# Kernel tuning notes

Hardware: AMD Instinct MI355X
Metric: run time of the kernel (lower is better)

The kernel has to match this reference:

```python
import jax, jax.numpy as jnp
import numpy as np

B, N, L = 32, 50, 16384  # batch, n_templates, segment length
KT = 4096                # template kernel length


def conv1d(x, w, pad, groups=1):
    # x: [B, Cin, L], w: [Cout, Cin/groups, K] (torch layout)
    return jax.lax.conv_general_dilated(
        x, w, window_strides=(1,), padding=[(pad, pad)],
        dimension_numbers=('NCH', 'OIH', 'NCH'), feature_group_count=groups)


def maxpool3(x):
    # MaxPool1d(kernel=3, stride=3), floor mode (VALID)
    return jax.lax.reduce_window(x, -jnp.inf, jax.lax.max,
                                 (1, 1, 3), (1, 1, 3), 'VALID')


def pad_to(x, m):
    p = (-x.shape[-1]) % m
    pads = ((0, 0),) * (x.ndim - 1) + ((0, p),)
    return jnp.pad(x, pads)


def setup_inputs() -> dict:
    key = jax.random.key(0)
    ks = jax.random.split(key, 12)
    return dict(
        xi=jax.random.normal(ks[0], (B, 2, L), jnp.float32),
        S_t_m12=jax.random.normal(ks[1], (2, 1, L), jnp.float32) * 0.01,
        template=jax.random.normal(ks[2], (N, 2, KT), jnp.float32) * 0.01,
        hh_sqrt=jax.random.uniform(ks[3], (N, 2), jnp.float32) + 0.5,
        W1=jax.random.normal(ks[4], (16, 2, 3), jnp.float32) * 0.1,
        b1=jnp.zeros((16,), jnp.float32),
        W2=jax.random.normal(ks[5], (32, 16, 3), jnp.float32) * 0.1,
        b2=jnp.zeros((32,), jnp.float32),
        W3=jax.random.normal(ks[6], (32, 128), jnp.float32) * 0.1,
        b3=jnp.zeros((32,), jnp.float32),
        W4=jax.random.normal(ks[7], (2, 32), jnp.float32) * 0.1,
        b4=jnp.zeros((2,), jnp.float32),
    )


def reference(xi, S_t_m12, template, hh_sqrt, W1, b1, W2, b2, W3, b3, W4, b4):
    # Whitening matched filter: grouped conv with kernel length L
    y = conv1d(xi, S_t_m12, L - 1, groups=2)          # [B, 2, 2L-1]
    y = pad_to(y, L)                                   # [B, 2, 2L]
    # wrap-fold each channel: reshape(B,2,L).sum over the fold axis
    d_SA = y[:, 0].reshape(-1, 2, L).sum(1)[:, None, :]  # [B,1,L]
    d_SE = y[:, 1].reshape(-1, 2, L).sum(1)[:, None, :]
    h_SA = template[:, 0, :].reshape(-1, 1, KT)          # [N,1,KT]
    h_SE = template[:, 1, :].reshape(-1, 1, KT)
    dh_A = pad_to(conv1d(d_SA, h_SA, KT - 1), L).reshape(-1, N, 2, L).sum(2)  # [B,N,L]
    dh_E = pad_to(conv1d(d_SE, h_SE, KT - 1), L).reshape(-1, N, 2, L).sum(2)
    z = jnp.stack((dh_A, dh_E), -1).transpose(0, 2, 1, 3)  # [B,L,N,2]
    z = z / hh_sqrt                                         # broadcast [N,2]
    z = z.max(axis=1).transpose(0, 2, 1)                    # [B,2,N]
    # small CNN + MLP head
    h = maxpool3(jax.nn.sigmoid(conv1d(z, W1, 0) + b1[None, :, None]))  # [B,16,16]
    h = maxpool3(jax.nn.sigmoid(conv1d(h, W2, 0) + b2[None, :, None]))  # [B,32,4]
    h = h.reshape(h.shape[0], -1)                                        # [B,128]
    h = jax.nn.relu(h @ W3.T + b3)
    return h @ W4.T + b4                                                 # [B,2]
```

## Files before the change

kernel.cpp:

```cpp
#include <hip/hip_runtime.h>
#include <math.h>

#define L_LEN 16384
#define M_LEN 8192
#define KT_LEN 4096
#define BB 32
#define NTPL 50
#define SPEC_STRIDE 8224
#define NSIG 166
#define NTF 1024
#define NTI 512
#define PI_F 3.14159265358979323846f
#define C8 0.92387953251128674f
#define S8 0.38268343236508978f
#define R2_F 0.70710678118654752f

typedef float cf2 __attribute__((ext_vector_type(2)));


__device__ __forceinline__ cf2 cmul(cf2 a, cf2 b) {
    cf2 t, d;
    asm("v_pk_mul_f32 %0, %1, %2 op_sel:[0,0] op_sel_hi:[0,1]"
        : "=v"(t) : "v"(a), "v"(b));
    asm("v_pk_fma_f32 %0, %1, %2, %3 op_sel:[1,1,0] op_sel_hi:[1,0,1] neg_lo:[0,1,0]"
        : "=v"(d) : "v"(a), "v"(b), "v"(t));
    return d;
}
__device__ __forceinline__ cf2 cmulc(cf2 a, cf2 b) {
    cf2 t, d;
    asm("v_pk_mul_f32 %0, %1, %2 op_sel:[0,0] op_sel_hi:[0,1] neg_hi:[0,1]"
        : "=v"(t) : "v"(a), "v"(b));
    asm("v_pk_fma_f32 %0, %1, %2, %3 op_sel:[1,1,0] op_sel_hi:[1,0,1]"
        : "=v"(d) : "v"(a), "v"(b), "v"(t));
    return d;
}
__device__ __forceinline__ cf2 cmulca(cf2 a, cf2 b) {
    cf2 t, d;
    asm("v_pk_mul_f32 %0, %1, %2 op_sel:[0,0] op_sel_hi:[0,1]"
        : "=v"(t) : "v"(a), "v"(b));
    asm("v_pk_fma_f32 %0, %1, %2, %3 op_sel:[1,1,0] op_sel_hi:[1,0,1] neg_hi:[1,0,0]"
        : "=v"(d) : "v"(a), "v"(b), "v"(t));
    return d;
}
__device__ __forceinline__ cf2 pk_addch(cf2 a, cf2 b) {
    cf2 d;
    asm("v_pk_add_f32 %0, %1, %2 neg_hi:[0,1]" : "=v"(d) : "v"(a), "v"(b));
    return d;
}
__device__ __forceinline__ cf2 pk_subcl(cf2 a, cf2 b) {
    cf2 d;
    asm("v_pk_add_f32 %0, %1, %2 neg_lo:[0,1]" : "=v"(d) : "v"(a), "v"(b));
    return d;
}
__device__ __forceinline__ cf2 pk_compose1(cf2 s, cf2 r) {
    cf2 d;
    asm("v_pk_add_f32 %0, %1, %2 op_sel:[0,1] op_sel_hi:[0,0] neg_lo:[0,1]"
        : "=v"(d) : "v"(s), "v"(r));
    return d;
}
__device__ __forceinline__ cf2 pk_compose2(cf2 s, cf2 r) {
    cf2 d;
    asm("v_pk_add_f32 %0, %1, %2 op_sel:[0,1] op_sel_hi:[0,0] neg_hi:[1,0]"
        : "=v"(d) : "v"(s), "v"(r));
    return d;
}
template<int SIGN>
__device__ __forceinline__ cf2 rot90(cf2 z) {
    return (SIGN < 0) ? (cf2){z.y, -z.x} : (cf2){-z.y, z.x};
}
template<int SIGN>
__device__ __forceinline__ cf2 ldT(const cf2* __restrict__ T, int idx) {
    cf2 t = T[idx];
    if (SIGN > 0) t.y = -t.y;
    return t;
}

__device__ __forceinline__ int swz(int i) { return i ^ (((i >> 5) & 15) << 1); }

__device__ __forceinline__ int pos8(int f) {
    return ((f & 7) << 10) | (((f >> 3) & 7) << 7) |
           (((f >> 6) & 7) << 4) | (((f >> 9) & 7) << 1) | ((f >> 12) & 1);
}

template<int SIGN>
__device__ __forceinline__ void dft16(cf2 x[16]) {
    const float S = (SIGN < 0) ? -1.f : 1.f;
    const cf2 w1 = {0.9238795325112867f, S * 0.3826834323650898f};
    const cf2 w2 = {0.7071067811865476f, S * 0.7071067811865476f};
    const cf2 w3 = {0.3826834323650898f, S * 0.9238795325112867f};
    cf2 v[16];
    #pragma unroll
    for (int n1 = 0; n1 < 4; ++n1) {
        cf2 a0 = x[n1], a1 = x[n1+4], a2 = x[n1+8], a3 = x[n1+12];
        cf2 t0 = a0 + a2, t2 = a0 - a2;
        cf2 t1 = a1 + a3, t3 = rot90<SIGN>(a1 - a3);
        cf2 u0 = t0 + t1, u1 = t2 + t3;
        cf2 u2 = t0 - t1, u3 = t2 - t3;
        if (n1 == 1) { u1 = cmul(u1, w1); u2 = cmul(u2, w2); u3 = cmul(u3, w3); }
        else if (n1 == 2) { u1 = cmul(u1, w2); u2 = rot90<SIGN>(u2);
                            u3 = rot90<SIGN>(cmul(u3, w2)); }
        else if (n1 == 3) { u1 = cmul(u1, w3); u2 = rot90<SIGN>(cmul(u2, w2));
                            u3 = -cmul(u3, w1); }
        v[0*4+n1] = u0; v[1*4+n1] = u1; v[2*4+n1] = u2; v[3*4+n1] = u3;
    }
    #pragma unroll
    for (int r = 0; r < 4; ++r) {
        cf2 a0 = v[r*4+0], a1 = v[r*4+1], a2 = v[r*4+2], a3 = v[r*4+3];
        cf2 t0 = a0 + a2, t2 = a0 - a2;
        cf2 t1 = a1 + a3, t3 = rot90<SIGN>(a1 - a3);
        x[r]    = t0 + t1; x[r+4]  = t2 + t3;
        x[r+8]  = t0 - t1; x[r+12] = t2 - t3;
    }
}

template<int SIGN>
__device__ __forceinline__ void butterfly16(cf2* A, const int idx[16], cf2 w1) {
    cf2 x[16];
    #pragma unroll
    for (int n = 0; n < 16; ++n) x[n] = A[idx[n]];
    dft16<SIGN>(x);
    A[idx[0]] = x[0];
    A[idx[1]] = cmul(x[1], w1);
    const cf2 w2 = cmul(w1, w1);
    A[idx[2]] = cmul(x[2], w2);
    const cf2 w3 = cmul(w1, w2);
    A[idx[3]] = cmul(x[3], w3);
    const cf2 w4 = cmul(w2, w2);
    A[idx[4]] = cmul(x[4], w4);
    A[idx[5]] = cmul(x[5], cmul(w1, w4));
    A[idx[6]] = cmul(x[6], cmul(w2, w4));
    A[idx[7]] = cmul(x[7], cmul(w3, w4));
    const cf2 w8 = cmul(w4, w4);
    A[idx[8]]  = cmul(x[8],  w8);
    A[idx[9]]  = cmul(x[9],  cmul(w1, w8));
    A[idx[10]] = cmul(x[10], cmul(w2, w8));
    A[idx[11]] = cmul(x[11], cmul(w3, w8));
    const cf2 w12 = cmul(w4, w8);
    A[idx[12]] = cmul(x[12], w12);
    A[idx[13]] = cmul(x[13], cmul(w1, w12));
    A[idx[14]] = cmul(x[14], cmul(w2, w12));
    A[idx[15]] = cmul(x[15], cmul(w3, w12));
}

template<int SIGN>
__device__ __forceinline__ void dft8(cf2 x[8]) {
    const cf2 w81 = { R2_F, SIGN * R2_F };
    const cf2 w83 = { -R2_F, SIGN * R2_F };
    cf2 u0 = x[0] + x[4], u1 = x[1] + x[5], u2 = x[2] + x[6], u3 = x[3] + x[7];
    cf2 v0 = x[0] - x[4];
    cf2 v1 = cmul(x[1] - x[5], w81);
    cf2 v2 = rot90<SIGN>(x[2] - x[6]);
    cf2 v3 = cmul(x[3] - x[7], w83);
    cf2 t0 = u0 + u2, t2 = u0 - u2;
    cf2 t1 = u1 + u3, t3 = rot90<SIGN>(u1 - u3);
    x[0] = t0 + t1; x[2] = t2 + t3; x[4] = t0 - t1; x[6] = t2 - t3;
    cf2 s0 = v0 + v2, s2 = v0 - v2;
    cf2 s1 = v1 + v3, s3 = rot90<SIGN>(v1 - v3);
    x[1] = s0 + s1; x[3] = s2 + s3; x[5] = s0 - s1; x[7] = s2 - s3;
}

template<int SIGN>
__device__ __forceinline__ void butterfly8(cf2* A, const int idx[8], cf2 w1) {
    cf2 x[8];
    #pragma unroll
    for (int n = 0; n < 8; ++n) x[n] = A[idx[n]];
    dft8<SIGN>(x);
    A[idx[0]] = x[0];
    A[idx[1]] = cmul(x[1], w1);
    const cf2 w2 = cmul(w1, w1);
    A[idx[2]] = cmul(x[2], w2);
    const cf2 w3 = cmul(w1, w2);
    A[idx[3]] = cmul(x[3], w3);
    const cf2 w4 = cmul(w2, w2);
    A[idx[4]] = cmul(x[4], w4);
    A[idx[5]] = cmul(x[5], cmul(w1, w4));
    A[idx[6]] = cmul(x[6], cmul(w2, w4));
    A[idx[7]] = cmul(x[7], cmul(w3, w4));
}

__global__ __launch_bounds__(NTF, 4)
void fwd_fft_kernel(const float* __restrict__ xi, const float* __restrict__ w,
                    const float* __restrict__ tmpl, cf2* __restrict__ Tw,
                    cf2* __restrict__ spec) {
    __shared__ __attribute__((aligned(16))) cf2 A[M_LEN];
    const int sig = blockIdx.x;
    const int tid = threadIdx.x;

    if (sig >= NSIG) {
        const int k = (sig - NSIG) * NTF + tid;
        const int quad = k >> 12, mm = k & 4095;
        float s, c; __sincosf(PI_F * (float)mm / 8192.f, &s, &c);
        cf2 v;
        if      (quad == 0) v = (cf2){ c, -s};
        else if (quad == 1) v = (cf2){-s, -c};
        else if (quad == 2) v = (cf2){-c,  s};
        else                v = (cf2){ s,  c};
        Tw[k] = v;
        return;
    }

    const float* src;
    int nre;
    if (sig < 64)      { src = xi   + sig * L_LEN;         nre = L_LEN; }
    else if (sig < 66) { src = w    + (sig - 64) * L_LEN;  nre = L_LEN; }
    else               { src = tmpl + (sig - 66) * KT_LEN; nre = KT_LEN; }
    const bool isW = (sig >= 64 && sig < 66);
    const int nc = nre >> 1;
    const float4* s4 = (const float4*)src;
    const int g0 = tid ^ ((tid >> 4) & 15);
    #pragma unroll
    for (int m = 0; m < 4; ++m) {
        const int u = 2*tid + 2048*m;
        float4 vv = (u < nc) ? s4[tid + 1024*m] : make_float4(0.f, 0.f, 0.f, 0.f);
        ((float4*)A)[g0 + 1024*m] = vv;
    }
    __syncthreads();

    {
        int idx[8]; const int b0 = swz(tid);
        #pragma unroll
        for (int n = 0; n < 8; ++n) idx[n] = b0 + 1024*n;
        float sn, cs; __sincosf(-PI_F * (float)(2*tid) / 8192.f, &sn, &cs);
        butterfly8<-1>(A, idx, (cf2){cs, sn});
    }
    __syncthreads();
    {
        const int blk = tid >> 7, j = tid & 127, jb = blk*1024;
        const int jsw = j ^ (((j >> 5) & 3) << 1);
        int idx[8];
        #pragma unroll
        for (int n = 0; n < 8; ++n) idx[n] = jb + 128*n + (jsw ^ ((n & 3) << 3));
        float sn, cs; __sincosf(-PI_F * (float)(16*j) / 8192.f, &sn, &cs);
        butterfly8<-1>(A, idx, (cf2){cs, sn});
    }
    __syncthreads();
    {
        const int blk = tid >> 4, j = tid & 15;
        const int base = blk*128 + j, bx = (blk & 3) << 3;
        int idx[8];
        #pragma unroll
        for (int n = 0; n < 8; ++n) idx[n] = (base + 16*n) ^ bx ^ ((n >> 1) << 1);
        float sn, cs; __sincosf(-PI_F * (float)(128*j) / 8192.f, &sn, &cs);
        butterfly8<-1>(A, idx, (cf2){cs, sn});
    }
    __syncthreads();
    {
        const int blk = tid >> 1, j = tid & 1;
        const int Xa = ((blk >> 1) & 15) << 1;
        const int base = ((blk << 4) | j) ^ (Xa & 16);
        const int xv = Xa & 14;
        int idx[8];
        #pragma unroll
        for (int n = 0; n < 8; ++n) idx[n] = base + ((2*n) ^ xv);
        cf2 w1 = j ? (cf2){C8, -S8} : (cf2){1.f, 0.f};
        butterfly8<-1>(A, idx, w1);
    }
    __syncthreads();
    #pragma unroll
    for (int m = 0; m < 4; ++m) {
        float4 pq = ((float4*)A)[g0 + 1024*m];
        ((float4*)A)[g0 + 1024*m] = make_float4(pq.x + pq.z, pq.y + pq.w,
                                                pq.x - pq.z, pq.y - pq.w);
    }
    __syncthreads();

    cf2* out = spec + (size_t)sig * SPEC_STRIDE;
    #pragma unroll
    for (int m = 0; m < 8; ++m) {
        const int f = tid + 1024*m;
        const int fb = (M_LEN - f) & (M_LEN - 1);
        cf2 Za = A[swz(pos8(f))];
        cf2 Zb = A[swz(pos8(fb))];
        cf2 E = (cf2){0.5f*(Za.x + Zb.x), 0.5f*(Za.y - Zb.y)};
        cf2 D = (cf2){Za.x - Zb.x, Za.y + Zb.y};
        cf2 O = (cf2){0.5f*D.y, -0.5f*D.x};
        float sn, cs;
        __sincosf(-PI_F * (float)f / 8192.f, &sn, &cs);
        cf2 val = E + (cf2){cs*O.x - sn*O.y, cs*O.y + sn*O.x};
        if (isW) {
            const int k = (4094 * f) & (L_LEN - 1);
            float psn, pcs; __sincosf(-PI_F * (float)k / 8192.f, &psn, &pcs);
            val = cmul((cf2){val.x, -val.y}, (cf2){pcs, psn});
        }
        out[f] = val;
    }
    if (tid == 0) {
        cf2 Za = A[swz(0)];
        cf2 val = (cf2){Za.x - Za.y, 0.f};
        if (isW) {
            val = (cf2){-val.x, 0.f};
        }
        out[M_LEN] = val;
    }
}

__global__ __launch_bounds__(1024)
void xv_kernel(cf2* __restrict__ spec) {
    const int bc = blockIdx.x;
    cf2* Xs = spec + (size_t)bc * SPEC_STRIDE;
    const cf2* Vs = spec + (size_t)(64 + (bc & 1)) * SPEC_STRIDE;
    const int tid = threadIdx.x;
    float4* X4 = (float4*)Xs;
    const float4* V4 = (const float4*)Vs;
    #pragma unroll
    for (int m = 0; m < 4; ++m) {
        const int p = tid + 1024*m;
        float4 xv = X4[p], vv = V4[p];
        cf2 a = cmul((cf2){xv.x, xv.y}, (cf2){vv.x, vv.y});
        cf2 b = cmul((cf2){xv.z, xv.w}, (cf2){vv.z, vv.w});
        X4[p] = make_float4(a.x, a.y, b.x, b.y);
    }
    if (tid == 0) Xs[M_LEN] = cmul(Xs[M_LEN], Vs[M_LEN]);
}

__global__ __launch_bounds__(NTI, 4)
void inv_fft_kernel(const cf2* __restrict__ spec, const cf2* __restrict__ T,
                    const float* __restrict__ hh, float* __restrict__ zarr) {
    __shared__ __attribute__((aligned(16))) cf2 A[M_LEN];
    const int idx0 = blockIdx.x;
    const int c = idx0 & 1;
    const int n = (idx0 >> 1) % NTPL;
    const int b = idx0 / (2 * NTPL);
    const int tid = threadIdx.x;

    const cf2* Xs = spec + (size_t)(b*2 + c)      * SPEC_STRIDE;
    const cf2* Hs = spec + (size_t)(66 + n*2 + c) * SPEC_STRIDE;
    const float4* X4 = (const float4*)Xs;
    const float4* H4 = (const float4*)Hs;
    const float4* T4 = (const float4*)T;

    #pragma unroll
    for (int m = 0; m < 2; ++m) {
        const int tp = tid + 512*m;
        const int f0 = 2*tp, f1 = f0 + 1;
        float4 xa = X4[tp],        ha = H4[tp];
        float4 xq = X4[tp + 2048], hq = H4[tp + 2048];
        cf2 PA0 = cmulc((cf2){xa.x, xa.y}, (cf2){ha.x, ha.y});
        cf2 PA1 = cmulc((cf2){xa.z, xa.w}, (cf2){ha.z, ha.w});
        cf2 QB0 = cmulc((cf2){xq.x, xq.y}, (cf2){hq.x, hq.y});
        cf2 QB1 = cmulc((cf2){xq.z, xq.w}, (cf2){hq.z, hq.w});
        cf2 PB0 = cmulc(Xs[4096 - f0], Hs[4096 - f0]);
        cf2 PB1 = cmulc(Xs[4096 - f1], Hs[4096 - f1]);
        cf2 QA0 = cmulc(Xs[8192 - f0], Hs[8192 - f0]);
        cf2 QA1 = cmulc(Xs[8192 - f1], Hs[8192 - f1]);
        float4 tf4 = T4[tp];
        float4 t2a = T4[2*tp];
        float4 t2b = T4[2*tp + 1];
        cf2 Tf0 = (cf2){tf4.x, tf4.y}, Tf1 = (cf2){tf4.z, tf4.w};
        cf2 T20 = (cf2){t2a.x, t2a.y}, T21 = (cf2){t2b.x, t2b.y};
        cf2 SpA0 = pk_addch(PA0, QA0), SmA0 = pk_subcl(PA0, QA0);
        cf2 RA0 = cmulca(Tf0, SmA0);
        cf2 ZA1_0 = pk_compose1(SpA0, RA0);
        cf2 ZA2_0 = pk_compose2(SpA0, RA0);
        cf2 tB0 = (cf2){-Tf0.y, -Tf0.x};
        cf2 SpB0 = pk_addch(PB0, QB0), SmB0 = pk_subcl(PB0, QB0);
        cf2 RB0 = cmulca(tB0, SmB0);
        cf2 ZB1_0 = pk_compose1(SpB0, RB0);
        cf2 ZB2_0 = pk_compose2(SpB0, RB0);
        cf2 top0 = ZA1_0 + ZB2_0;
        cf2 bot0 = cmulca(T20, ZA1_0 - ZB2_0);
        cf2 SpA1 = pk_addch(PA1, QA1), SmA1 = pk_subcl(PA1, QA1);
        cf2 RA1 = cmulca(Tf1, SmA1);
        cf2 ZA1_1 = pk_compose1(SpA1, RA1);
        cf2 ZA2_1 = pk_compose2(SpA1, RA1);
        cf2 tB1 = (cf2){-Tf1.y, -Tf1.x};
        cf2 SpB1 = pk_addch(PB1, QB1), SmB1 = pk_subcl(PB1, QB1);
        cf2 RB1 = cmulca(tB1, SmB1);
        cf2 ZB1_1 = pk_compose1(SpB1, RB1);
        cf2 ZB2_1 = pk_compose2(SpB1, RB1);
        cf2 top1 = ZA1_1 + ZB2_1;
        cf2 bot1 = cmulca(T21, ZA1_1 - ZB2_1);
        const int gt = tp ^ ((tp >> 4) & 15);
        ((float4*)A)[gt]        = make_float4(top0.x, top0.y, top1.x, top1.y);
        ((float4*)A)[2048 + gt] = make_float4(bot0.x, bot0.y, bot1.x, bot1.y);
        if (tp > 0) {
            cf2 tr0 = ZB1_0 + ZA2_0;
            cf2 dr0 = cmul(ZB1_0 - ZA2_0, T20);
            A[swz(4096 - f0)] = tr0;
            A[swz(8192 - f0)] = -dr0;
        }
        cf2 tr1 = ZB1_1 + ZA2_1;
        cf2 dr1 = cmul(ZB1_1 - ZA2_1, T21);
        A[swz(4096 - f1)] = tr1;
        A[swz(8192 - f1)] = -dr1;
    }
    if (tid == 0) {
        cf2 P = cmulc(Xs[2048], Hs[2048]);
        cf2 Q = cmulc(Xs[6144], Hs[6144]);
        cf2 Tc = (cf2){R2_F, -R2_F};
        cf2 Sp = pk_addch(P, Q), Sm = pk_subcl(P, Q);
        cf2 R = cmulca(Tc, Sm);
        cf2 Z1 = pk_compose1(Sp, R), Z2 = pk_compose2(Sp, R);
        cf2 d = Z1 - Z2;
        A[swz(2048)] = Z1 + Z2;
        A[swz(6144)] = (cf2){-d.y, d.x};
    }
    __syncthreads();

    {
        const int h = tid >> 8, j = tid & 255;
        const int Hb = h << 12;
        const int jx = j ^ (((j >> 5) & 7) << 1);
        int idx[16];
        #pragma unroll
        for (int nn = 0; nn < 16; ++nn)
            idx[nn] = Hb + 256*nn + (jx ^ ((nn & 1) << 4));
        butterfly16<+1>(A, idx, ldT<+1>(T, 4*j));
    }
    __syncthreads();
    {
        const int h = tid >> 8, q = (tid >> 4) & 15, j = tid & 15;
        const int base = (h << 12) + (q << 8);
        const int qb = q & 1;
        int idx[16];
        #pragma unroll
        for (int nn = 0; nn < 16; ++nn)
            idx[nn] = base + 16*(nn ^ qb) + (j ^ (((nn >> 1) & 7) << 1));
        butterfly16<+1>(A, idx, ldT<+1>(T, 64*j));
    }
    __syncthreads();

    float mx = -INFINITY;
    {
        const int bb = 16 * (tid ^ ((tid >> 4) & 1));
        const int m3 = ((tid >> 1) & 7) << 1;
        cf2 x[16];
        #pragma unroll
        for (int e = 0; e < 8; ++e) {
            float4 v = ((const float4*)A)[(bb + ((2*e) ^ m3)) >> 1];
            x[2*e]     = (cf2){v.x, v.y};
            x[2*e + 1] = (cf2){v.z, v.w};
        }
        dft16<+1>(x);
        #pragma unroll
        for (int nn = 0; nn < 16; ++nn)
            mx = fmaxf(mx, fmaxf(x[nn].x, x[nn].y));
    }
    __syncthreads();
    for (int off = 32; off > 0; off >>= 1)
        mx = fmaxf(mx, __shfl_xor(mx, off));
    const int lane = tid & 63, wv = tid >> 6;
    float* redf = (float*)A;
    if (lane == 0) redf[wv] = mx;
    __syncthreads();
    if (tid == 0) {
        float mm = redf[0];
        for (int i = 1; i < NTI/64; ++i) mm = fmaxf(mm, redf[i]);
        zarr[(b*2 + c)*NTPL + n] = mm / (2.f * (float)M_LEN * hh[n*2 + c]);
    }
}

#define W1_OFF 0
#define B1_OFF 96
#define W2_OFF 112
#define B2_OFF 1648
#define W3_OFF 1680
#define B3_OFF 5904
#define W4_OFF 5936
#define B4_OFF 6000
#define WSM_SZ 6002

__global__ __launch_bounds__(256)
void head_kernel(const float* __restrict__ zarr,
                 const float* __restrict__ W1, const float* __restrict__ b1,
                 const float* __restrict__ W2, const float* __restrict__ b2,
                 const float* __restrict__ W3, const float* __restrict__ b3,
                 const float* __restrict__ W4, const float* __restrict__ b4,
                 float* __restrict__ out) {
    __shared__ float wsm[WSM_SZ];
    __shared__ float zl[2*NTPL];
    __shared__ float s1[16*48];
    __shared__ float p1[16*16];
    __shared__ float s2[32*14];
    __shared__ float hflat[128];
    __shared__ float h1[32];
    const int b = blockIdx.x, tid = threadIdx.x;

    for (int i = tid; i < 96;   i += 256) wsm[W1_OFF + i] = W1[i];
    if (tid < 16)                         wsm[B1_OFF + tid] = b1[tid];
    for (int i = tid; i < 1536; i += 256) wsm[W2_OFF + i] = W2[i];
    if (tid < 32)                         wsm[B2_OFF + tid] = b2[tid];
    for (int i = tid; i < 4096; i += 256)
        wsm[W3_OFF + (i >> 7)*132 + (i & 127)] = W3[i];
    if (tid < 32)                         wsm[B3_OFF + tid] = b3[tid];
    if (tid < 64)                         wsm[W4_OFF + tid] = W4[tid];
    if (tid < 2)                          wsm[B4_OFF + tid] = b4[tid];
    for (int i = tid; i < 2*NTPL; i += 256) zl[i] = zarr[b*2*NTPL + i];
    __syncthreads();

    for (int i = tid; i < 16*48; i += 256) {
        const int o = i / 48, t = i % 48;
        float acc = wsm[B1_OFF + o];
        #pragma unroll
        for (int cc = 0; cc < 2; ++cc)
            #pragma unroll
            for (int k = 0; k < 3; ++k)
                acc += zl[cc*NTPL + t + k] * wsm[W1_OFF + o*6 + cc*3 + k];
        s1[i] = 1.f / (1.f + __expf(-acc));
    }
    __syncthreads();
    for (int i = tid; i < 16*16; i += 256) {
        const int o = i / 16, u = i % 16;
        p1[i] = fmaxf(fmaxf(s1[o*48 + 3*u], s1[o*48 + 3*u+1]), s1[o*48 + 3*u+2]);
    }
    __syncthreads();
    for (int i = tid; i < 32*14; i += 256) {
        const int o = i / 14, t = i % 14;
        float acc = wsm[B2_OFF + o];
        #pragma unroll
        for (int cc = 0; cc < 16; ++cc)
            #pragma unroll
            for (int k = 0; k < 3; ++k)
                acc += p1[cc*16 + t + k] * wsm[W2_OFF + o*48 + cc*3 + k];
        s2[o*14 + t] = 1.f / (1.f + __expf(-acc));
    }
    __syncthreads();
    for (int i = tid; i < 128; i += 256) {
        const int o = i / 4, u = i % 4;
        hflat[i] = fmaxf(fmaxf(s2[o*14 + 3*u], s2[o*14 + 3*u+1]), s2[o*14 + 3*u+2]);
    }
    __syncthreads();
    {
        const int o = tid >> 3, lg = tid & 7;
        float acc = 0.f;
        #pragma unroll
        for (int k = 0; k < 16; ++k)
            acc += hflat[lg + 8*k] * wsm[W3_OFF + o*132 + lg + 8*k];
        acc += __shfl_xor(acc, 1);
        acc += __shfl_xor(acc, 2);
        acc += __shfl_xor(acc, 4);
        if (lg == 0) h1[o] = fmaxf(acc + wsm[B3_OFF + o], 0.f);
    }
    __syncthreads();
    if (tid < 64) {
        const int o = tid >> 5, j = tid & 31;
        float p = h1[j] * wsm[W4_OFF + o*32 + j];
        p += __shfl_xor(p, 1);
        p += __shfl_xor(p, 2);
        p += __shfl_xor(p, 4);
        p += __shfl_xor(p, 8);
        p += __shfl_xor(p, 16);
        if (j == 0) out[b*2 + o] = p + wsm[B4_OFF + o];
    }
}

extern "C" void kernel_launch(void* const* d_in, const int* in_sizes, int n_in,
                              void* d_out, int out_size, void* d_ws, size_t ws_size,
                              hipStream_t stream) {
    const float* xi   = (const float*)d_in[0];
    const float* Sw   = (const float*)d_in[1];
    const float* tmpl = (const float*)d_in[2];
    const float* hh   = (const float*)d_in[3];
    const float* W1   = (const float*)d_in[4];
    const float* b1   = (const float*)d_in[5];
    const float* W2   = (const float*)d_in[6];
    const float* b2   = (const float*)d_in[7];
    const float* W3   = (const float*)d_in[8];
    const float* b3   = (const float*)d_in[9];
    const float* W4   = (const float*)d_in[10];
    const float* b4   = (const float*)d_in[11];
    float* out = (float*)d_out;

    cf2* T16  = (cf2*)d_ws;
    cf2* spec = T16 + 16384;
    float* zarr = (float*)(spec + (size_t)NSIG * SPEC_STRIDE);

    fwd_fft_kernel<<<dim3(NSIG + 16), dim3(NTF), 0, stream>>>(xi, Sw, tmpl, T16, spec);
    xv_kernel<<<dim3(64), dim3(1024), 0, stream>>>(spec);
    inv_fft_kernel<<<dim3(BB * NTPL * 2), dim3(NTI), 0, stream>>>(spec, T16, hh, zarr);
    head_kernel<<<dim3(BB), dim3(256), 0, stream>>>(zarr, W1, b1, W2, b2, W3, b3, W4, b4, out);
}
```

Baseline: 152.0 us.

## Split forward 8192-point FFT into two 4096-point halves per block

The forward FFT kernel now does a first decimation-in-frequency radix-2 step while loading from global memory. It then splits each signal's 8192-point complex FFT into even and odd halves, each computed by a separate 256-thread block as a 4096-point FFT with three radix-16 passes. This doubles the block count and shrinks LDS per block from 64KB to 32KB, aiming for better occupancy and fewer barrier stages. The cost is that each block re-reads the full input, plus extra twiddle sincos work on the odd half.

```diff
diff --git a/kernel.cpp b/kernel.cpp
--- a/kernel.cpp
+++ b/kernel.cpp
@@ -8,12 +8,11 @@
 #define NTPL 50
 #define SPEC_STRIDE 8224
 #define NSIG 166
-#define NTF 1024
 #define NTI 512
 #define PI_F 3.14159265358979323846f
-#define C8 0.92387953251128674f
-#define S8 0.38268343236508978f
 #define R2_F 0.70710678118654752f
+#define CW1 0.99999970586288223f
+#define SW1 7.6699031874270453e-4f
 
 typedef float cf2 __attribute__((ext_vector_type(2)));
 
@@ -77,9 +76,8 @@
 
 __device__ __forceinline__ int swz(int i) { return i ^ (((i >> 5) & 15) << 1); }
 
-__device__ __forceinline__ int pos8(int f) {
-    return ((f & 7) << 10) | (((f >> 3) & 7) << 7) |
-           (((f >> 6) & 7) << 4) | (((f >> 9) & 7) << 1) | ((f >> 12) & 1);
+__device__ __forceinline__ int pos4(int f) {
+    return ((f & 15) << 8) | (f & 0xF0) | ((f >> 8) & 15);
 }
 
 template<int SIGN>
@@ -142,52 +140,16 @@
     A[idx[15]] = cmul(x[15], cmul(w3, w12));
 }
 
-template<int SIGN>
-__device__ __forceinline__ void dft8(cf2 x[8]) {
-    const cf2 w81 = { R2_F, SIGN * R2_F };
-    const cf2 w83 = { -R2_F, SIGN * R2_F };
-    cf2 u0 = x[0] + x[4], u1 = x[1] + x[5], u2 = x[2] + x[6], u3 = x[3] + x[7];
-    cf2 v0 = x[0] - x[4];
-    cf2 v1 = cmul(x[1] - x[5], w81);
-    cf2 v2 = rot90<SIGN>(x[2] - x[6]);
-    cf2 v3 = cmul(x[3] - x[7], w83);
-    cf2 t0 = u0 + u2, t2 = u0 - u2;
-    cf2 t1 = u1 + u3, t3 = rot90<SIGN>(u1 - u3);
-    x[0] = t0 + t1; x[2] = t2 + t3; x[4] = t0 - t1; x[6] = t2 - t3;
-    cf2 s0 = v0 + v2, s2 = v0 - v2;
-    cf2 s1 = v1 + v3, s3 = rot90<SIGN>(v1 - v3);
-    x[1] = s0 + s1; x[3] = s2 + s3; x[5] = s0 - s1; x[7] = s2 - s3;
-}
-
-template<int SIGN>
-__device__ __forceinline__ void butterfly8(cf2* A, const int idx[8], cf2 w1) {
-    cf2 x[8];
-    #pragma unroll
-    for (int n = 0; n < 8; ++n) x[n] = A[idx[n]];
-    dft8<SIGN>(x);
-    A[idx[0]] = x[0];
-    A[idx[1]] = cmul(x[1], w1);
-    const cf2 w2 = cmul(w1, w1);
-    A[idx[2]] = cmul(x[2], w2);
-    const cf2 w3 = cmul(w1, w2);
-    A[idx[3]] = cmul(x[3], w3);
-    const cf2 w4 = cmul(w2, w2);
-    A[idx[4]] = cmul(x[4], w4);
-    A[idx[5]] = cmul(x[5], cmul(w1, w4));
-    A[idx[6]] = cmul(x[6], cmul(w2, w4));
-    A[idx[7]] = cmul(x[7], cmul(w3, w4));
-}
-
-__global__ __launch_bounds__(NTF, 4)
+__global__ __launch_bounds__(256, 4)
 void fwd_fft_kernel(const float* __restrict__ xi, const float* __restrict__ w,
                     const float* __restrict__ tmpl, cf2* __restrict__ Tw,
                     cf2* __restrict__ spec) {
-    __shared__ __attribute__((aligned(16))) cf2 A[M_LEN];
-    const int sig = blockIdx.x;
+    __shared__ __attribute__((aligned(16))) cf2 A[4096];
+    const int hb = blockIdx.x;
     const int tid = threadIdx.x;
 
-    if (sig >= NSIG) {
-        const int k = (sig - NSIG) * NTF + tid;
+    if (hb >= 2*NSIG) {
+        const int k = (hb - 2*NSIG) * 256 + tid;
         const int quad = k >> 12, mm = k & 4095;
         float s, c; __sincosf(PI_F * (float)mm / 8192.f, &s, &c);
         cf2 v;
@@ -199,78 +161,83 @@
         return;
     }
 
+    const int sig = hb >> 1, half = hb & 1;
     const float* src;
     int nre;
     if (sig < 64)      { src = xi   + sig * L_LEN;         nre = L_LEN; }
     else if (sig < 66) { src = w    + (sig - 64) * L_LEN;  nre = L_LEN; }
     else               { src = tmpl + (sig - 66) * KT_LEN; nre = KT_LEN; }
     const bool isW = (sig >= 64 && sig < 66);
-    const int nc = nre >> 1;
+    const int nf4 = nre >> 2;
     const float4* s4 = (const float4*)src;
-    const int g0 = tid ^ ((tid >> 4) & 15);
-    #pragma unroll
-    for (int m = 0; m < 4; ++m) {
-        const int u = 2*tid + 2048*m;
-        float4 vv = (u < nc) ? s4[tid + 1024*m] : make_float4(0.f, 0.f, 0.f, 0.f);
-        ((float4*)A)[g0 + 1024*m] = vv;
-    }
-    __syncthreads();
-
-    {
-        int idx[8]; const int b0 = swz(tid);
-        #pragma unroll
-        for (int n = 0; n < 8; ++n) idx[n] = b0 + 1024*n;
-        float sn, cs; __sincosf(-PI_F * (float)(2*tid) / 8192.f, &sn, &cs);
-        butterfly8<-1>(A, idx, (cf2){cs, sn});
-    }
-    __syncthreads();
-    {
-        const int blk = tid >> 7, j = tid & 127, jb = blk*1024;
-        const int jsw = j ^ (((j >> 5) & 3) << 1);
-        int idx[8];
-        #pragma unroll
-        for (int n = 0; n < 8; ++n) idx[n] = jb + 128*n + (jsw ^ ((n & 3) << 3));
-        float sn, cs; __sincosf(-PI_F * (float)(16*j) / 8192.f, &sn, &cs);
-        butterfly8<-1>(A, idx, (cf2){cs, sn});
-    }
-    __syncthreads();
-    {
-        const int blk = tid >> 4, j = tid & 15;
-        const int base = blk*128 + j, bx = (blk & 3) << 3;
-        int idx[8];
-        #pragma unroll
-        for (int n = 0; n < 8; ++n) idx[n] = (base + 16*n) ^ bx ^ ((n >> 1) << 1);
-        float sn, cs; __sincosf(-PI_F * (float)(128*j) / 8192.f, &sn, &cs);
-        butterfly8<-1>(A, idx, (cf2){cs, sn});
-    }
-    __syncthreads();
-    {
-        const int blk = tid >> 1, j = tid & 1;
-        const int Xa = ((blk >> 1) & 15) << 1;
-        const int base = ((blk << 4) | j) ^ (Xa & 16);
-        const int xv = Xa & 14;
-        int idx[8];
-        #pragma unroll
-        for (int n = 0; n < 8; ++n) idx[n] = base + ((2*n) ^ xv);
-        cf2 w1 = j ? (cf2){C8, -S8} : (cf2){1.f, 0.f};
-        butterfly8<-1>(A, idx, w1);
-    }
-    __syncthreads();
-    #pragma unroll
-    for (int m = 0; m < 4; ++m) {
-        float4 pq = ((float4*)A)[g0 + 1024*m];
-        ((float4*)A)[g0 + 1024*m] = make_float4(pq.x + pq.z, pq.y + pq.w,
-                                                pq.x - pq.z, pq.y - pq.w);
+
+    const cf2 w1c = (cf2){CW1, -SW1};
+    #pragma unroll
+    for (int mm = 0; mm < 8; ++mm) {
+        const int j = tid + 256*mm;
+        float4 a = (j < nf4)        ? s4[j]        : make_float4(0.f,0.f,0.f,0.f);
+        float4 b = (j + 2048 < nf4) ? s4[j + 2048] : make_float4(0.f,0.f,0.f,0.f);
+        cf2 c0 = (cf2){a.x, a.y}, c1 = (cf2){a.z, a.w};
+        cf2 d0 = (cf2){b.x, b.y}, d1 = (cf2){b.z, b.w};
+        cf2 h0, h1;
+        if (half == 0) { h0 = c0 + d0; h1 = c1 + d1; }
+        else {
+            float sn, cs; __sincosf(-PI_F * (float)j / 2048.f, &sn, &cs);
+            cf2 wk = (cf2){cs, sn};
+            h0 = cmul(c0 - d0, wk);
+            h1 = cmul(c1 - d1, cmul(wk, w1c));
+        }
+        const int g = j ^ ((j >> 4) & 15);
+        ((float4*)A)[g] = make_float4(h0.x, h0.y, h1.x, h1.y);
+    }
+    __syncthreads();
+
+    {
+        const int jx = tid ^ (((tid >> 5) & 7) << 1);
+        int idx[16];
+        #pragma unroll
+        for (int n = 0; n < 16; ++n) idx[n] = (jx ^ ((n & 1) << 4)) + 256*n;
+        float sn, cs; __sincosf(-PI_F * (float)tid / 2048.f, &sn, &cs);
+        butterfly16<-1>(A, idx, (cf2){cs, sn});
+    }
+    __syncthreads();
+    {
+        const int q = tid >> 4, j = tid & 15;
+        const int base = q << 8, qb = q & 1;
+        int idx[16];
+        #pragma unroll
+        for (int n = 0; n < 16; ++n)
+            idx[n] = base + 16*(n ^ qb) + (j ^ (((n >> 1) & 7) << 1));
+        float sn, cs; __sincosf(-PI_F * (float)j / 128.f, &sn, &cs);
+        butterfly16<-1>(A, idx, (cf2){cs, sn});
+    }
+    __syncthreads();
+    {
+        const int bb = 16 * (tid ^ ((tid >> 4) & 1));
+        const int m3 = ((tid >> 1) & 7) << 1;
+        cf2 x[16];
+        #pragma unroll
+        for (int e = 0; e < 8; ++e) {
+            float4 v = ((const float4*)A)[(bb + ((2*e) ^ m3)) >> 1];
+            x[2*e]     = (cf2){v.x, v.y};
+            x[2*e + 1] = (cf2){v.z, v.w};
+        }
+        dft16<-1>(x);
+        #pragma unroll
+        for (int e = 0; e < 8; ++e)
+            ((float4*)A)[(bb + ((2*e) ^ m3)) >> 1] =
+                make_float4(x[2*e].x, x[2*e].y, x[2*e+1].x, x[2*e+1].y);
     }
     __syncthreads();
 
     cf2* out = spec + (size_t)sig * SPEC_STRIDE;
     #pragma unroll
-    for (int m = 0; m < 8; ++m) {
-        const int f = tid + 1024*m;
-        const int fb = (M_LEN - f) & (M_LEN - 1);
-        cf2 Za = A[swz(pos8(f))];
-        cf2 Zb = A[swz(pos8(fb))];
+    for (int mm = 0; mm < 16; ++mm) {
+        const int m = tid + 256*mm;
+        const int mb = half ? (4095 - m) : ((4096 - m) & 4095);
+        const int f = 2*m + half;
+        cf2 Za = A[swz(pos4(m))];
+        cf2 Zb = A[swz(pos4(mb))];
         cf2 E = (cf2){0.5f*(Za.x + Zb.x), 0.5f*(Za.y - Zb.y)};
         cf2 D = (cf2){Za.x - Zb.x, Za.y + Zb.y};
         cf2 O = (cf2){0.5f*D.y, -0.5f*D.x};
@@ -284,8 +251,8 @@
         }
         out[f] = val;
     }
-    if (tid == 0) {
-        cf2 Za = A[swz(0)];
+    if (half == 0 && tid == 0) {
+        cf2 Za = A[0];
         cf2 val = (cf2){Za.x - Za.y, 0.f};
         if (isW) {
             val = (cf2){-val.x, 0.f};
@@ -565,7 +532,7 @@
     cf2* spec = T16 + 16384;
     float* zarr = (float*)(spec + (size_t)NSIG * SPEC_STRIDE);
 
-    fwd_fft_kernel<<<dim3(NSIG + 16), dim3(NTF), 0, stream>>>(xi, Sw, tmpl, T16, spec);
+    fwd_fft_kernel<<<dim3(2*NSIG + 64), dim3(256), 0, stream>>>(xi, Sw, tmpl, T16, spec);
     xv_kernel<<<dim3(64), dim3(1024), 0, stream>>>(spec);
     inv_fft_kernel<<<dim3(BB * NTPL * 2), dim3(NTI), 0, stream>>>(spec, T16, hh, zarr);
     head_kernel<<<dim3(BB), dim3(256), 0, stream>>>(zarr, W1, b1, W2, b2, W3, b3, W4, b4, out);
```

Result: slower. 155.4 us (+2.2%).
